# Performance work log

Measured on AMD Instinct MI355X. Metric: run time of the kernel, lower is better.

The kernel has to match this reference:

```python
import jax, jax.numpy as jnp
import numpy as np

TOP_K = 2
E = 8      # num_experts
D = 1024   # model dim
F = 2048   # expert hidden dim = int(2*3072/3), already a multiple of 256
B, S = 2, 1024


def setup_inputs() -> dict:
    key = jax.random.key(0)
    ks = jax.random.split(key, 8)
    sc = 0.02
    return {
        "x_bsD": jax.random.normal(ks[0], (B, S, D), dtype=jnp.float32),
        "router_DE": jax.random.normal(ks[1], (D, E), dtype=jnp.float32) * sc,
        "w_in_shared_FD": jax.random.normal(ks[2], (F, D), dtype=jnp.float32) * sc,
        "w_out_shared_DF": jax.random.normal(ks[3], (D, F), dtype=jnp.float32) * sc,
        "w_swiglu_FD": jax.random.normal(ks[4], (F, D), dtype=jnp.float32) * sc,
        "w_in_eDF": jax.random.normal(ks[5], (E, D, F), dtype=jnp.float32) * sc,
        "w_swiglu_eDF": jax.random.normal(ks[6], (E, D, F), dtype=jnp.float32) * sc,
        "w_out_eFD": jax.random.normal(ks[7], (E, F, D), dtype=jnp.float32) * sc,
    }


def reference(x_bsD, router_DE, w_in_shared_FD, w_out_shared_DF, w_swiglu_FD,
              w_in_eDF, w_swiglu_eDF, w_out_eFD):
    b, s, d = x_bsD.shape
    x_aD = x_bsD.reshape(-1, d)                      # [a, D]
    a = x_aD.shape[0]

    # Router (token choice): top-k per token, others masked to -inf
    scores_aE = x_aD @ router_DE                      # [a, E]
    topv_aK, topi_aK = jax.lax.top_k(scores_aE, TOP_K)
    masked_aE = jnp.full_like(scores_aE, -jnp.inf)
    masked_aE = masked_aE.at[jnp.arange(a)[:, None], topi_aK].set(topv_aK)
    # sigmoid(-inf) == 0 -> non-selected (expert, token) pairs contribute nothing
    gates_Ea = jax.nn.sigmoid(masked_aE.astype(jnp.float32)).astype(x_aD.dtype).T  # [E, a]

    # Dispatch: router_indices_EG == arange(a) per expert, so gather == broadcast
    routed_in_EaD = x_aD[None, :, :] * gates_Ea[:, :, None]   # [E, a, D]
    routed_in_EaD = jax.lax.stop_gradient(routed_in_EaD)      # matches .detach()

    # Per-expert bmm SwiGLU
    mid_EaF = jnp.einsum('ead,edf->eaf', routed_in_EaD, w_in_eDF)
    sw_EaF = jnp.einsum('ead,edf->eaf', routed_in_EaD, w_swiglu_eDF)
    h_EaF = jax.nn.silu(mid_EaF) * sw_EaF
    out_EaD = jnp.einsum('eaf,efd->ead', h_EaF, w_out_eFD)

    # Shared expert (computed under torch.no_grad in the original)
    shared_aF = jax.nn.silu(x_aD @ w_in_shared_FD.T) * (x_aD @ w_swiglu_FD.T)
    shared_out_aD = jax.lax.stop_gradient(shared_aF @ w_out_shared_DF.T)

    # Combine: scatter_add with per-expert arange indices == sum over experts
    out_aD = shared_out_aD + jnp.sum(out_EaD, axis=0)
    return out_aD.reshape(b, s, d)
```

## Files before the change

### kernel.cpp

```cpp
#include <hip/hip_runtime.h>
#include <hip/hip_bf16.h>

#define A_TOK 2048
#define DDIM 1024
#define FDIM 2048
#define NEXP 8
#define NE9 9
#define SLOTS_R (2 * A_TOK)
#define SLOTS_T (SLOTS_R + A_TOK)
#define NB1 (2 * FDIM)

#define PREP_TRA_END 4096
#define PREP_SH12_END (PREP_TRA_END + 1024)
#define PREP_SHOUT_END (PREP_SH12_END + 512)
#define PREP_NWG (PREP_SHOUT_END + 512)

typedef __attribute__((ext_vector_type(8))) short short8v;
typedef __attribute__((ext_vector_type(4))) float f32x4;
typedef __attribute__((ext_vector_type(4))) ushort ushort4v;

#define BARRIER() asm volatile("s_barrier" ::: "memory")
#define VMCNT(n) asm volatile("s_waitcnt vmcnt(" #n ")" ::: "memory")

__device__ __forceinline__ void lds16(const void* g, void* l) {
  __builtin_amdgcn_global_load_lds((const __attribute__((address_space(1))) void*)g,
                                   (__attribute__((address_space(3))) void*)l, 16, 0, 0);
}

__device__ __forceinline__ float sigmoidf_(float x) { return 1.f / (1.f + __expf(-x)); }
__device__ __forceinline__ ushort f2bf(float x) {
  __hip_bfloat16 b = __float2bfloat16(x);
  ushort u; __builtin_memcpy(&u, &b, 2); return u;
}
__device__ __forceinline__ float bf2f(ushort u) {
  union { unsigned int i; float f; } x; x.i = (unsigned int)u << 16; return x.f;
}

__global__ void k_prep(const float* __restrict__ w_in_e, const float* __restrict__ w_sw_e,
                       const float* __restrict__ w_in_sh, const float* __restrict__ w_sw_sh,
                       const float* __restrict__ w_out_sh,
                       ushort* __restrict__ wt12, ushort* __restrict__ wt_out_t,
                       const float* __restrict__ x, const float* __restrict__ rw,
                       __hip_bfloat16* __restrict__ xbf, int* __restrict__ top_e,
                       float* __restrict__ top_g) {
  __shared__ ushort tile[128][68];
  int b = blockIdx.x, tid = threadIdx.x;
  if (b < PREP_TRA_END) {
    int z = b >> 8, p = b & 255;
    int e = z & 7, which = z >> 3;
    const float* in = (which ? w_sw_e : w_in_e) + (size_t)e * DDIM * FDIM;
    ushort* outb = wt12 + (size_t)e * NB1 * DDIM;
    int r0 = (p & 7) * 128, c0 = (p >> 3) * 64;
    int rr = tid >> 4, cq = tid & 15;
    float4 va[8];
#pragma unroll
    for (int i = 0; i < 8; i++)
      va[i] = *(const float4*)(in + (size_t)(r0 + i * 16 + rr) * FDIM + c0 + cq * 4);
#pragma unroll
    for (int i = 0; i < 8; i++) {
      float4 v = va[i];
      ushort4v o = {f2bf(v.x), f2bf(v.y), f2bf(v.z), f2bf(v.w)};
      *(ushort4v*)&tile[i * 16 + rr][cq * 4] = o;
    }
    __syncthreads();
    int cc = tid >> 5, rq = tid & 31;
#pragma unroll
    for (int i = 0; i < 8; i++) {
      int c = i * 8 + cc;
      int f = c0 + c;
      int rp = ((f >> 5) << 6) + (which << 5) + (f & 31);
      ushort4v o = {tile[rq * 4 + 0][c], tile[rq * 4 + 1][c],
                    tile[rq * 4 + 2][c], tile[rq * 4 + 3][c]};
      *(ushort4v*)(outb + (size_t)rp * DDIM + r0 + rq * 4) = o;
    }
  } else if (b < PREP_SH12_END) {
    int j = b - PREP_TRA_END;
    int rj = j * 4 + (tid >> 6);
    int l = tid & 63;
    int which = rj & 1, f = rj >> 1;
    const float* src = (which ? w_sw_sh : w_in_sh) + (size_t)f * DDIM;
    int rp = ((f >> 5) << 6) + (which << 5) + (f & 31);
    ushort* dst = wt12 + (size_t)NEXP * NB1 * DDIM + (size_t)rp * DDIM;
#pragma unroll
    for (int i = 0; i < 4; i++) {
      int q = l + 64 * i;
      float4 v = ((const float4*)src)[q];
      ushort4v o = {f2bf(v.x), f2bf(v.y), f2bf(v.z), f2bf(v.w)};
      ((ushort4v*)dst)[q] = o;
    }
  } else if (b < PREP_SHOUT_END) {
    int j = b - PREP_SH12_END;
    int d = j * 2 + (tid >> 7);
    int l = tid & 127;
    const float* src = w_out_sh + (size_t)d * FDIM;
    ushort* dst = wt_out_t + (size_t)NEXP * DDIM * FDIM + (size_t)d * FDIM;
#pragma unroll
    for (int i = 0; i < 4; i++) {
      int q = l + 128 * i;
      float4 v = ((const float4*)src)[q];
      ushort4v o = {f2bf(v.x), f2bf(v.y), f2bf(v.z), f2bf(v.w)};
      ((ushort4v*)dst)[q] = o;
    }
  } else {
    int j = b - PREP_SHOUT_END;
    int t = j * 4 + (tid >> 6);
    int l = tid & 63;
    const float* xr = x + (size_t)t * DDIM;
    float acc[NEXP];
#pragma unroll
    for (int e = 0; e < NEXP; e++) acc[e] = 0.f;
#pragma unroll
    for (int i = 0; i < 16; i++) {
      int d = i * 64 + l;
      float v = xr[d];
      xbf[(size_t)t * DDIM + d] = __float2bfloat16(v);
      const float* rr = rw + (size_t)d * NEXP;
#pragma unroll
      for (int e = 0; e < NEXP; e++) acc[e] += v * rr[e];
    }
#pragma unroll
    for (int e = 0; e < NEXP; e++) {
#pragma unroll
      for (int s = 32; s > 0; s >>= 1) acc[e] += __shfl_xor(acc[e], s);
    }
    if (l == 0) {
      float b1 = -1e30f, b2 = -1e30f;
      int i1 = 0, i2 = 0;
#pragma unroll
      for (int e = 0; e < NEXP; e++) {
        float v = acc[e];
        if (v > b1) { b2 = b1; i2 = i1; b1 = v; i1 = e; }
        else if (v > b2) { b2 = v; i2 = e; }
      }
      top_e[t * 2 + 0] = i1; top_e[t * 2 + 1] = i2;
      top_g[t * 2 + 0] = sigmoidf_(b1); top_g[t * 2 + 1] = sigmoidf_(b2);
    }
  }
}

__global__ void k_scan(const int* __restrict__ top_e, int* __restrict__ counts,
                       int* __restrict__ offs, int* __restrict__ cursor) {
  __shared__ int hist[NEXP];
  int tid = threadIdx.x;
  if (tid < NEXP) hist[tid] = 0;
  __syncthreads();
  for (int i = tid; i < A_TOK * 2; i += 256) atomicAdd(&hist[top_e[i]], 1);
  __syncthreads();
  if (tid == 0) {
    int s = 0;
    for (int e = 0; e < NEXP; e++) { counts[e] = hist[e]; offs[e] = s; s += hist[e]; cursor[e] = 0; }
    counts[NEXP] = A_TOK;
    offs[NEXP] = s;
  }
}

__global__ void k_dispatch(const float* __restrict__ x, const int* __restrict__ top_e,
                           const float* __restrict__ top_g, const int* __restrict__ offs,
                           int* __restrict__ cursor, int* __restrict__ slot_of,
                           __hip_bfloat16* __restrict__ y) {
  int t = blockIdx.x * 4 + (threadIdx.x >> 6);
  int l = threadIdx.x & 63;
  int e0 = top_e[t * 2 + 0], e1 = top_e[t * 2 + 1];
  float g0 = top_g[t * 2 + 0], g1 = top_g[t * 2 + 1];
  int s0 = 0, s1 = 0;
  if (l == 0) {
    s0 = offs[e0] + atomicAdd(&cursor[e0], 1);
    s1 = offs[e1] + atomicAdd(&cursor[e1], 1);
    slot_of[t * 2 + 0] = s0; slot_of[t * 2 + 1] = s1;
  }
  s0 = __shfl(s0, 0); s1 = __shfl(s1, 0);
  const float* xr = x + (size_t)t * DDIM;
#pragma unroll
  for (int i = 0; i < 16; i++) {
    int d = i * 64 + l;
    float v = xr[d];
    y[(size_t)s0 * DDIM + d] = __float2bfloat16(v * g0);
    y[(size_t)s1 * DDIM + d] = __float2bfloat16(v * g1);
  }
}

__global__ __launch_bounds__(256, 3) void k_mlp1(
    const ushort* __restrict__ Abase, const ushort* __restrict__ Bbase,
    ushort* __restrict__ Obase, const int* __restrict__ d_cnt,
    const int* __restrict__ d_off, const float* __restrict__ w_out_e,
    ushort* __restrict__ wt_out_t) {
  constexpr int K = DDIM, NT = DDIM / 32;
  constexpr int BUF = 16384;
  __shared__ __align__(16) char smem[3 * BUF];
  int z = blockIdx.z;
  int tid = threadIdx.x;
  if (z < 4) {
    ushort (*tile)[68] = (ushort(*)[68])smem;
    int jj = (z * 16 + blockIdx.y) * 32 + blockIdx.x;
    int ex = jj >> 8, p = jj & 255;
    const float* in = w_out_e + (size_t)ex * FDIM * DDIM;
    ushort* outp = wt_out_t + (size_t)ex * DDIM * FDIM;
    int r0 = (p >> 4) * 128, c0 = (p & 15) * 64;
    int rr = tid >> 4, cq = tid & 15;
    float4 va[8];
#pragma unroll
    for (int i = 0; i < 8; i++)
      va[i] = *(const float4*)(in + (size_t)(r0 + i * 16 + rr) * DDIM + c0 + cq * 4);
#pragma unroll
    for (int i = 0; i < 8; i++) {
      float4 v = va[i];
      ushort4v o = {f2bf(v.x), f2bf(v.y), f2bf(v.z), f2bf(v.w)};
      *(ushort4v*)&tile[i * 16 + rr][cq * 4] = o;
    }
    __syncthreads();
    int cc = tid >> 5, rq = tid & 31;
#pragma unroll
    for (int i = 0; i < 8; i++) {
      int c = i * 8 + cc;
      ushort4v o = {tile[rq * 4 + 0][c], tile[rq * 4 + 1][c],
                    tile[rq * 4 + 2][c], tile[rq * 4 + 3][c]};
      *(ushort4v*)(outp + (size_t)(c0 + c) * FDIM + r0 + rq * 4) = o;
    }
    return;
  }
  int e = z - 4;
  int cnt = d_cnt[e];
  int m0 = blockIdx.y * 128;
  if (m0 >= cnt) return;
  int roff = d_off[e];
  int n0 = blockIdx.x * 128;
  const ushort* B = Bbase + (size_t)e * NB1 * DDIM;
  int w = tid >> 6, l = tid & 63;
  int wm = w >> 1, wn = w & 1, lr = l & 15, kg = l >> 4;
  size_t arow0 = (size_t)roff + m0;

  int srow = tid >> 2;
  int sgg = (tid & 3) ^ ((tid >> 3) & 3);
  const ushort* pA0 = Abase + (arow0 + srow) * (size_t)K + sgg * 8;
  const ushort* pA1 = pA0 + (size_t)64 * K;
  const ushort* pB0 = B + ((size_t)n0 + srow) * K + sgg * 8;
  const ushort* pB1 = pB0 + (size_t)64 * K;
  int tls = tid * 16;

  int xorg = (kg ^ ((lr >> 1) & 3)) << 4;
  int offA[4], offB[4];
#pragma unroll
  for (int i = 0; i < 4; i++) {
    offA[i] = (wm * 64 + i * 16 + lr) * 64 + xorg;
    offB[i] = 8192 + (wn * 64 + i * 16 + lr) * 64 + xorg;
  }

  f32x4 acc[4][4];
#pragma unroll
  for (int i = 0; i < 4; i++)
#pragma unroll
    for (int j = 0; j < 4; j++) acc[i][j] = {0.f, 0.f, 0.f, 0.f};

#pragma unroll
  for (int pt = 0; pt < 2; ++pt) {
    char* bb = smem + pt * BUF;
    lds16(pA0, bb + tls);         pA0 += 32;
    lds16(pA1, bb + 4096 + tls);  pA1 += 32;
    lds16(pB0, bb + 8192 + tls);  pB0 += 32;
    lds16(pB1, bb + 12288 + tls); pB1 += 32;
  }
  VMCNT(4);
  BARRIER();

  char* b0 = smem;
  char* b1 = smem + BUF;
  char* b2 = smem + 2 * BUF;
  for (int t = 0; t < NT; ++t) {
    bool st = (t + 2) < NT;
    short8v af[4], bf[4];
#pragma unroll
    for (int mf = 0; mf < 4; mf++) af[mf] = *(const short8v*)(b0 + offA[mf]);
#pragma unroll
    for (int nf = 0; nf < 2; nf++) bf[nf] = *(const short8v*)(b0 + offB[nf]);
    if (st) {
      lds16(pA0, b2 + tls);
      lds16(pA1, b2 + 4096 + tls);
    }
    pA0 += 32; pA1 += 32;
    BARRIER();
    __builtin_amdgcn_s_setprio(1);
#pragma unroll
    for (int nf = 0; nf < 2; nf++)
#pragma unroll
      for (int mf = 0; mf < 4; mf++)
        acc[mf][nf] = __builtin_amdgcn_mfma_f32_16x16x32_bf16(af[mf], bf[nf], acc[mf][nf], 0, 0, 0);
    __builtin_amdgcn_s_setprio(0);
    BARRIER();
#pragma unroll
    for (int nf = 2; nf < 4; nf++) bf[nf] = *(const short8v*)(b0 + offB[nf]);
    if (st) {
      lds16(pB0, b2 + 8192 + tls);
      lds16(pB1, b2 + 12288 + tls);
    }
    pB0 += 32; pB1 += 32;
    BARRIER();
    __builtin_amdgcn_s_setprio(1);
#pragma unroll
    for (int nf = 2; nf < 4; nf++)
#pragma unroll
      for (int mf = 0; mf < 4; mf++)
        acc[mf][nf] = __builtin_amdgcn_mfma_f32_16x16x32_bf16(af[mf], bf[nf], acc[mf][nf], 0, 0, 0);
    __builtin_amdgcn_s_setprio(0);
    if (t < NT - 1) {
      if (st) { VMCNT(4); } else { VMCNT(0); }
      BARRIER();
    }
    char* tmp = b0; b0 = b1; b1 = b2; b2 = tmp;
  }

  int j = (n0 >> 6) + wn;
#pragma unroll
  for (int mf = 0; mf < 4; mf++)
#pragma unroll
    for (int nf = 0; nf < 2; nf++)
#pragma unroll
      for (int r = 0; r < 4; r++) {
        int row = m0 + wm * 64 + mf * 16 + kg * 4 + r;
        if (row < cnt) {
          float mid = acc[mf][nf][r];
          float sw = acc[mf][nf + 2][r];
          float hv = mid * sigmoidf_(mid) * sw;
          int col = j * 32 + nf * 16 + lr;
          Obase[((size_t)roff + row) * FDIM + col] = f2bf(hv);
        }
      }
}

__global__ __launch_bounds__(256, 3) void k_mlp2(
    const ushort* __restrict__ Abase, const ushort* __restrict__ Bbase,
    ushort* __restrict__ part, const int* __restrict__ d_cnt,
    const int* __restrict__ d_off) {
  constexpr int K = FDIM, NT = 1024 / 32;
  constexpr int BUF = 16384;
  __shared__ __align__(16) char smem[3 * BUF];
  int e = blockIdx.z;
  int cnt = d_cnt[e];
  int mt = blockIdx.y >> 1, kz = blockIdx.y & 1;
  int m0 = mt * 128;
  if (m0 >= cnt) return;
  int roff = d_off[e];
  int n0 = blockIdx.x * 128;
  int kbeg = kz * 1024;
  const ushort* B = Bbase + (size_t)e * DDIM * FDIM;
  int tid = threadIdx.x, w = tid >> 6, l = tid & 63;
  int wm = w >> 1, wn = w & 1, lr = l & 15, kg = l >> 4;
  size_t arow0 = (size_t)roff + m0;

  int srow = tid >> 2;
  int sgg = (tid & 3) ^ ((tid >> 3) & 3);
  const ushort* pA0 = Abase + (arow0 + srow) * (size_t)K + kbeg + sgg * 8;
  const ushort* pA1 = pA0 + (size_t)64 * K;
  const ushort* pB0 = B + ((size_t)n0 + srow) * K + kbeg + sgg * 8;
  const ushort* pB1 = pB0 + (size_t)64 * K;
  int tls = tid * 16;

  int xorg = (kg ^ ((lr >> 1) & 3)) << 4;
  int offA[4], offB[4];
#pragma unroll
  for (int i = 0; i < 4; i++) {
    offA[i] = (wm * 64 + i * 16 + lr) * 64 + xorg;
    offB[i] = 8192 + (wn * 64 + i * 16 + lr) * 64 + xorg;
  }

  f32x4 acc[4][4];
#pragma unroll
  for (int i = 0; i < 4; i++)
#pragma unroll
    for (int j = 0; j < 4; j++) acc[i][j] = {0.f, 0.f, 0.f, 0.f};

#pragma unroll
  for (int pt = 0; pt < 2; ++pt) {
    char* bb = smem + pt * BUF;
    lds16(pA0, bb + tls);         pA0 += 32;
    lds16(pA1, bb + 4096 + tls);  pA1 += 32;
    lds16(pB0, bb + 8192 + tls);  pB0 += 32;
    lds16(pB1, bb + 12288 + tls); pB1 += 32;
  }
  VMCNT(4);
  BARRIER();

  char* b0 = smem;
  char* b1 = smem + BUF;
  char* b2 = smem + 2 * BUF;
  for (int t = 0; t < NT; ++t) {
    bool st = (t + 2) < NT;
    short8v af[4], bf[4];
#pragma unroll
    for (int mf = 0; mf < 4; mf++) af[mf] = *(const short8v*)(b0 + offA[mf]);
#pragma unroll
    for (int nf = 0; nf < 2; nf++) bf[nf] = *(const short8v*)(b0 + offB[nf]);
    if (st) {
      lds16(pA0, b2 + tls);
      lds16(pA1, b2 + 4096 + tls);
    }
    pA0 += 32; pA1 += 32;
    BARRIER();
    __builtin_amdgcn_s_setprio(1);
#pragma unroll
    for (int nf = 0; nf < 2; nf++)
#pragma unroll
      for (int mf = 0; mf < 4; mf++)
        acc[mf][nf] = __builtin_amdgcn_mfma_f32_16x16x32_bf16(af[mf], bf[nf], acc[mf][nf], 0, 0, 0);
    __builtin_amdgcn_s_setprio(0);
    BARRIER();
#pragma unroll
    for (int nf = 2; nf < 4; nf++) bf[nf] = *(const short8v*)(b0 + offB[nf]);
    if (st) {
      lds16(pB0, b2 + 8192 + tls);
      lds16(pB1, b2 + 12288 + tls);
    }
    pB0 += 32; pB1 += 32;
    BARRIER();
    __builtin_amdgcn_s_setprio(1);
#pragma unroll
    for (int nf = 2; nf < 4; nf++)
#pragma unroll
      for (int mf = 0; mf < 4; mf++)
        acc[mf][nf] = __builtin_amdgcn_mfma_f32_16x16x32_bf16(af[mf], bf[nf], acc[mf][nf], 0, 0, 0);
    __builtin_amdgcn_s_setprio(0);
    if (t < NT - 1) {
      if (st) { VMCNT(4); } else { VMCNT(0); }
      BARRIER();
    }
    char* tmp = b0; b0 = b1; b1 = b2; b2 = tmp;
  }

  ushort* outp = part + (size_t)kz * SLOTS_T * DDIM;
#pragma unroll
  for (int mf = 0; mf < 4; mf++)
#pragma unroll
    for (int nf = 0; nf < 4; nf++)
#pragma unroll
      for (int r = 0; r < 4; r++) {
        int row = m0 + wm * 64 + mf * 16 + kg * 4 + r;
        if (row < cnt) {
          int col = n0 + wn * 64 + nf * 16 + lr;
          outp[((size_t)roff + row) * DDIM + col] = f2bf(acc[mf][nf][r]);
        }
      }
}

__global__ void k_combine(const ushort* __restrict__ part, const int* __restrict__ slot_of,
                          float* __restrict__ out) {
  int t = blockIdx.x, q = threadIdx.x;
  int rows[3];
  rows[0] = slot_of[t * 2 + 0];
  rows[1] = slot_of[t * 2 + 1];
  rows[2] = SLOTS_R + t;
  size_t P = (size_t)SLOTS_T * DDIM;
  float o[4] = {0.f, 0.f, 0.f, 0.f};
#pragma unroll
  for (int kz = 0; kz < 2; kz++)
#pragma unroll
    for (int i = 0; i < 3; i++) {
      ushort4v v = *(const ushort4v*)(part + kz * P + (size_t)rows[i] * DDIM + q * 4);
#pragma unroll
      for (int j = 0; j < 4; j++) o[j] += bf2f(v[j]);
    }
  float4 ov = {o[0], o[1], o[2], o[3]};
  ((float4*)out)[(size_t)t * (DDIM / 4) + q] = ov;
}

extern "C" void kernel_launch(void* const* d_in, const int* in_sizes, int n_in,
                              void* d_out, int out_size, void* d_ws, size_t ws_size,
                              hipStream_t stream) {
  (void)in_sizes; (void)n_in; (void)out_size; (void)ws_size;
  const float* x        = (const float*)d_in[0];
  const float* router   = (const float*)d_in[1];
  const float* w_in_sh  = (const float*)d_in[2];
  const float* w_out_sh = (const float*)d_in[3];
  const float* w_sw_sh  = (const float*)d_in[4];
  const float* w_in_e   = (const float*)d_in[5];
  const float* w_sw_e   = (const float*)d_in[6];
  const float* w_out_e  = (const float*)d_in[7];
  float* out = (float*)d_out;

  char* ws = (char*)d_ws;
  size_t off = 0;
  auto alloc = [&](size_t bytes) -> char* {
    char* p = ws + off;
    off += (bytes + 255) & ~(size_t)255;
    return p;
  };
  ushort* wt12     = (ushort*)alloc((size_t)NE9 * NB1 * DDIM * 2);
  ushort* wt_out_t = (ushort*)alloc((size_t)NE9 * DDIM * FDIM * 2);
  __hip_bfloat16* y_all = (__hip_bfloat16*)alloc((size_t)SLOTS_R * DDIM * 2);
  __hip_bfloat16* xbf   = (__hip_bfloat16*)alloc((size_t)A_TOK * DDIM * 2);
  ushort* h        = (ushort*)alloc((size_t)SLOTS_T * FDIM * 2);
  int*   counts  = (int*)alloc(64);
  int*   offs    = (int*)alloc(64);
  int*   cursor  = (int*)alloc(64);
  int*   top_e   = (int*)alloc((size_t)A_TOK * 2 * 4);
  float* top_g   = (float*)alloc((size_t)A_TOK * 2 * 4);
  int*   slot_of = (int*)alloc((size_t)A_TOK * 2 * 4);
  (void)alloc(1 << 20);
  ushort* part = wt12;

  k_prep<<<dim3(PREP_NWG), 256, 0, stream>>>(
      w_in_e, w_sw_e, w_in_sh, w_sw_sh, w_out_sh,
      wt12, wt_out_t, x, router, xbf, top_e, top_g);

  k_scan<<<dim3(1), 256, 0, stream>>>(top_e, counts, offs, cursor);

  k_dispatch<<<dim3(A_TOK / 4), 256, 0, stream>>>(x, top_e, top_g, offs, cursor, slot_of, y_all);

  k_mlp1<<<dim3(NB1 / 128, A_TOK / 128, 4 + NE9), 256, 0, stream>>>(
      (const ushort*)y_all, wt12, h, counts, offs, w_out_e, wt_out_t);

  k_mlp2<<<dim3(DDIM / 128, (A_TOK / 128) * 2, NE9), 256, 0, stream>>>(
      h, wt_out_t, part, counts, offs);

  k_combine<<<dim3(A_TOK), 256, 0, stream>>>(part, slot_of, out);
}
```

Baseline: 248.9 us.

## Retile expert up-projection GEMM to 128x256 with 64-wide K steps

The expert up-projection kernel moves from 128x128 tiles with 256 threads and 32-wide K steps to 128x256 tiles with 512 threads (8 waves) and 64-wide K steps. It keeps triple-buffered LDS at 48KB per stage and uses a new 8-way XOR swizzle. The w_out_e fp32-to-bf16 transpose moves out of the GEMM launch into the prep kernel, so the GEMM grid no longer carries extra non-GEMM blocks. The goal is more reuse per byte loaded into LDS and fewer barriers per unit of K. In exchange, the ~144KB of LDS limits each CU to a single block, and the larger tile leaves fewer blocks to spread across CUs.

```diff
diff --git a/kernel.cpp b/kernel.cpp
--- a/kernel.cpp
+++ b/kernel.cpp
@@ -11,7 +11,8 @@
 #define NB1 (2 * FDIM)
 
 #define PREP_TRA_END 4096
-#define PREP_SH12_END (PREP_TRA_END + 1024)
+#define PREP_TRB_END (PREP_TRA_END + 2048)
+#define PREP_SH12_END (PREP_TRB_END + 1024)
 #define PREP_SHOUT_END (PREP_SH12_END + 512)
 #define PREP_NWG (PREP_SHOUT_END + 512)
 
@@ -37,8 +38,8 @@
 }
 
 __global__ void k_prep(const float* __restrict__ w_in_e, const float* __restrict__ w_sw_e,
-                       const float* __restrict__ w_in_sh, const float* __restrict__ w_sw_sh,
-                       const float* __restrict__ w_out_sh,
+                       const float* __restrict__ w_out_e, const float* __restrict__ w_in_sh,
+                       const float* __restrict__ w_sw_sh, const float* __restrict__ w_out_sh,
                        ushort* __restrict__ wt12, ushort* __restrict__ wt_out_t,
                        const float* __restrict__ x, const float* __restrict__ rw,
                        __hip_bfloat16* __restrict__ xbf, int* __restrict__ top_e,
@@ -73,8 +74,34 @@
                     tile[rq * 4 + 2][c], tile[rq * 4 + 3][c]};
       *(ushort4v*)(outb + (size_t)rp * DDIM + r0 + rq * 4) = o;
     }
+  } else if (b < PREP_TRB_END) {
+    int b2 = b - PREP_TRA_END;
+    int ex = b2 >> 8, p = b2 & 255;
+    const float* in = w_out_e + (size_t)ex * FDIM * DDIM;
+    ushort* outp = wt_out_t + (size_t)ex * DDIM * FDIM;
+    int r0 = (p >> 4) * 128, c0 = (p & 15) * 64;
+    int rr = tid >> 4, cq = tid & 15;
+    float4 va[8];
+#pragma unroll
+    for (int i = 0; i < 8; i++)
+      va[i] = *(const float4*)(in + (size_t)(r0 + i * 16 + rr) * DDIM + c0 + cq * 4);
+#pragma unroll
+    for (int i = 0; i < 8; i++) {
+      float4 v = va[i];
+      ushort4v o = {f2bf(v.x), f2bf(v.y), f2bf(v.z), f2bf(v.w)};
+      *(ushort4v*)&tile[i * 16 + rr][cq * 4] = o;
+    }
+    __syncthreads();
+    int cc = tid >> 5, rq = tid & 31;
+#pragma unroll
+    for (int i = 0; i < 8; i++) {
+      int c = i * 8 + cc;
+      ushort4v o = {tile[rq * 4 + 0][c], tile[rq * 4 + 1][c],
+                    tile[rq * 4 + 2][c], tile[rq * 4 + 3][c]};
+      *(ushort4v*)(outp + (size_t)(c0 + c) * FDIM + r0 + rq * 4) = o;
+    }
   } else if (b < PREP_SH12_END) {
-    int j = b - PREP_TRA_END;
+    int j = b - PREP_TRB_END;
     int rj = j * 4 + (tid >> 6);
     int l = tid & 63;
     int which = rj & 1, f = rj >> 1;
@@ -179,71 +206,42 @@
   }
 }
 
-__global__ __launch_bounds__(256, 3) void k_mlp1(
+__global__ __launch_bounds__(512, 1) void k_mlp1(
     const ushort* __restrict__ Abase, const ushort* __restrict__ Bbase,
     ushort* __restrict__ Obase, const int* __restrict__ d_cnt,
-    const int* __restrict__ d_off, const float* __restrict__ w_out_e,
-    ushort* __restrict__ wt_out_t) {
-  constexpr int K = DDIM, NT = DDIM / 32;
-  constexpr int BUF = 16384;
+    const int* __restrict__ d_off) {
+  constexpr int K = DDIM, NT = DDIM / 64;
+  constexpr int ABUF = 16384, BUF = 49152;
   __shared__ __align__(16) char smem[3 * BUF];
-  int z = blockIdx.z;
-  int tid = threadIdx.x;
-  if (z < 4) {
-    ushort (*tile)[68] = (ushort(*)[68])smem;
-    int jj = (z * 16 + blockIdx.y) * 32 + blockIdx.x;
-    int ex = jj >> 8, p = jj & 255;
-    const float* in = w_out_e + (size_t)ex * FDIM * DDIM;
-    ushort* outp = wt_out_t + (size_t)ex * DDIM * FDIM;
-    int r0 = (p >> 4) * 128, c0 = (p & 15) * 64;
-    int rr = tid >> 4, cq = tid & 15;
-    float4 va[8];
-#pragma unroll
-    for (int i = 0; i < 8; i++)
-      va[i] = *(const float4*)(in + (size_t)(r0 + i * 16 + rr) * DDIM + c0 + cq * 4);
-#pragma unroll
-    for (int i = 0; i < 8; i++) {
-      float4 v = va[i];
-      ushort4v o = {f2bf(v.x), f2bf(v.y), f2bf(v.z), f2bf(v.w)};
-      *(ushort4v*)&tile[i * 16 + rr][cq * 4] = o;
-    }
-    __syncthreads();
-    int cc = tid >> 5, rq = tid & 31;
-#pragma unroll
-    for (int i = 0; i < 8; i++) {
-      int c = i * 8 + cc;
-      ushort4v o = {tile[rq * 4 + 0][c], tile[rq * 4 + 1][c],
-                    tile[rq * 4 + 2][c], tile[rq * 4 + 3][c]};
-      *(ushort4v*)(outp + (size_t)(c0 + c) * FDIM + r0 + rq * 4) = o;
-    }
-    return;
-  }
-  int e = z - 4;
+  int e = blockIdx.z;
   int cnt = d_cnt[e];
   int m0 = blockIdx.y * 128;
   if (m0 >= cnt) return;
   int roff = d_off[e];
-  int n0 = blockIdx.x * 128;
+  int n0 = blockIdx.x * 256;
   const ushort* B = Bbase + (size_t)e * NB1 * DDIM;
-  int w = tid >> 6, l = tid & 63;
-  int wm = w >> 1, wn = w & 1, lr = l & 15, kg = l >> 4;
+  int tid = threadIdx.x, w = tid >> 6, l = tid & 63;
+  int wm = w >> 2, wn = w & 3, lr = l & 15, kg = l >> 4;
   size_t arow0 = (size_t)roff + m0;
 
-  int srow = tid >> 2;
-  int sgg = (tid & 3) ^ ((tid >> 3) & 3);
-  const ushort* pA0 = Abase + (arow0 + srow) * (size_t)K + sgg * 8;
+  int srow = tid >> 3;
+  int sg = (tid & 7) ^ (srow & 7);
+  const ushort* pA0 = Abase + (arow0 + srow) * (size_t)K + sg * 8;
   const ushort* pA1 = pA0 + (size_t)64 * K;
-  const ushort* pB0 = B + ((size_t)n0 + srow) * K + sgg * 8;
+  const ushort* pB0 = B + ((size_t)n0 + srow) * K + sg * 8;
   const ushort* pB1 = pB0 + (size_t)64 * K;
+  const ushort* pB2 = pB0 + (size_t)128 * K;
+  const ushort* pB3 = pB0 + (size_t)192 * K;
   int tls = tid * 16;
 
-  int xorg = (kg ^ ((lr >> 1) & 3)) << 4;
   int offA[4], offB[4];
 #pragma unroll
   for (int i = 0; i < 4; i++) {
-    offA[i] = (wm * 64 + i * 16 + lr) * 64 + xorg;
-    offB[i] = 8192 + (wn * 64 + i * 16 + lr) * 64 + xorg;
-  }
+    offA[i] = (wm * 64 + i * 16 + lr) * 128;
+    offB[i] = ABUF + (wn * 64 + i * 16 + lr) * 128;
+  }
+  int sk0 = (kg ^ (lr & 7)) << 4;
+  int sk1 = ((4 + kg) ^ (lr & 7)) << 4;
 
   f32x4 acc[4][4];
 #pragma unroll
@@ -254,12 +252,14 @@
 #pragma unroll
   for (int pt = 0; pt < 2; ++pt) {
     char* bb = smem + pt * BUF;
-    lds16(pA0, bb + tls);         pA0 += 32;
-    lds16(pA1, bb + 4096 + tls);  pA1 += 32;
-    lds16(pB0, bb + 8192 + tls);  pB0 += 32;
-    lds16(pB1, bb + 12288 + tls); pB1 += 32;
-  }
-  VMCNT(4);
+    lds16(pA0, bb + tls);                pA0 += 64;
+    lds16(pA1, bb + 8192 + tls);         pA1 += 64;
+    lds16(pB0, bb + ABUF + tls);         pB0 += 64;
+    lds16(pB1, bb + ABUF + 8192 + tls);  pB1 += 64;
+    lds16(pB2, bb + ABUF + 16384 + tls); pB2 += 64;
+    lds16(pB3, bb + ABUF + 24576 + tls); pB3 += 64;
+  }
+  VMCNT(6);
   BARRIER();
 
   char* b0 = smem;
@@ -269,14 +269,11 @@
     bool st = (t + 2) < NT;
     short8v af[4], bf[4];
 #pragma unroll
-    for (int mf = 0; mf < 4; mf++) af[mf] = *(const short8v*)(b0 + offA[mf]);
-#pragma unroll
-    for (int nf = 0; nf < 2; nf++) bf[nf] = *(const short8v*)(b0 + offB[nf]);
-    if (st) {
-      lds16(pA0, b2 + tls);
-      lds16(pA1, b2 + 4096 + tls);
-    }
-    pA0 += 32; pA1 += 32;
+    for (int i = 0; i < 4; i++) af[i] = *(const short8v*)(b0 + offA[i] + sk0);
+    bf[0] = *(const short8v*)(b0 + offB[0] + sk0);
+    bf[1] = *(const short8v*)(b0 + offB[1] + sk0);
+    if (st) { lds16(pA0, b2 + tls); lds16(pA1, b2 + 8192 + tls); }
+    pA0 += 64; pA1 += 64;
     BARRIER();
     __builtin_amdgcn_s_setprio(1);
 #pragma unroll
@@ -286,13 +283,10 @@
         acc[mf][nf] = __builtin_amdgcn_mfma_f32_16x16x32_bf16(af[mf], bf[nf], acc[mf][nf], 0, 0, 0);
     __builtin_amdgcn_s_setprio(0);
     BARRIER();
-#pragma unroll
-    for (int nf = 2; nf < 4; nf++) bf[nf] = *(const short8v*)(b0 + offB[nf]);
-    if (st) {
-      lds16(pB0, b2 + 8192 + tls);
-      lds16(pB1, b2 + 12288 + tls);
-    }
-    pB0 += 32; pB1 += 32;
+    bf[2] = *(const short8v*)(b0 + offB[2] + sk0);
+    bf[3] = *(const short8v*)(b0 + offB[3] + sk0);
+    if (st) { lds16(pB0, b2 + ABUF + tls); lds16(pB1, b2 + ABUF + 8192 + tls); }
+    pB0 += 64; pB1 += 64;
     BARRIER();
     __builtin_amdgcn_s_setprio(1);
 #pragma unroll
@@ -301,10 +295,34 @@
       for (int mf = 0; mf < 4; mf++)
         acc[mf][nf] = __builtin_amdgcn_mfma_f32_16x16x32_bf16(af[mf], bf[nf], acc[mf][nf], 0, 0, 0);
     __builtin_amdgcn_s_setprio(0);
-    if (t < NT - 1) {
-      if (st) { VMCNT(4); } else { VMCNT(0); }
-      BARRIER();
-    }
+    BARRIER();
+#pragma unroll
+    for (int i = 0; i < 4; i++) af[i] = *(const short8v*)(b0 + offA[i] + sk1);
+    bf[0] = *(const short8v*)(b0 + offB[0] + sk1);
+    bf[1] = *(const short8v*)(b0 + offB[1] + sk1);
+    if (st) { lds16(pB2, b2 + ABUF + 16384 + tls); lds16(pB3, b2 + ABUF + 24576 + tls); }
+    pB2 += 64; pB3 += 64;
+    BARRIER();
+    __builtin_amdgcn_s_setprio(1);
+#pragma unroll
+    for (int nf = 0; nf < 2; nf++)
+#pragma unroll
+      for (int mf = 0; mf < 4; mf++)
+        acc[mf][nf] = __builtin_amdgcn_mfma_f32_16x16x32_bf16(af[mf], bf[nf], acc[mf][nf], 0, 0, 0);
+    __builtin_amdgcn_s_setprio(0);
+    BARRIER();
+    bf[2] = *(const short8v*)(b0 + offB[2] + sk1);
+    bf[3] = *(const short8v*)(b0 + offB[3] + sk1);
+    if (st) { VMCNT(6); } else { VMCNT(0); }
+    BARRIER();
+    __builtin_amdgcn_s_setprio(1);
+#pragma unroll
+    for (int nf = 2; nf < 4; nf++)
+#pragma unroll
+      for (int mf = 0; mf < 4; mf++)
+        acc[mf][nf] = __builtin_amdgcn_mfma_f32_16x16x32_bf16(af[mf], bf[nf], acc[mf][nf], 0, 0, 0);
+    __builtin_amdgcn_s_setprio(0);
+    BARRIER();
     char* tmp = b0; b0 = b1; b1 = b2; b2 = tmp;
   }
 
@@ -497,15 +515,15 @@
   ushort* part = wt12;
 
   k_prep<<<dim3(PREP_NWG), 256, 0, stream>>>(
-      w_in_e, w_sw_e, w_in_sh, w_sw_sh, w_out_sh,
+      w_in_e, w_sw_e, w_out_e, w_in_sh, w_sw_sh, w_out_sh,
       wt12, wt_out_t, x, router, xbf, top_e, top_g);
 
   k_scan<<<dim3(1), 256, 0, stream>>>(top_e, counts, offs, cursor);
 
   k_dispatch<<<dim3(A_TOK / 4), 256, 0, stream>>>(x, top_e, top_g, offs, cursor, slot_of, y_all);
 
-  k_mlp1<<<dim3(NB1 / 128, A_TOK / 128, 4 + NE9), 256, 0, stream>>>(
-      (const ushort*)y_all, wt12, h, counts, offs, w_out_e, wt_out_t);
+  k_mlp1<<<dim3(NB1 / 256, A_TOK / 128, NE9), 512, 0, stream>>>(
+      (const ushort*)y_all, wt12, h, counts, offs);
 
   k_mlp2<<<dim3(DDIM / 128, (A_TOK / 128) * 2, NE9), 256, 0, stream>>>(
       h, wt_out_t, part, counts, offs);
```

New measurement: 259.8 us. 1.04x slower.

## Move w_out transpose into prep kernel and remap block orders for XCD locality

Applied to the files above, without the earlier changes.

Moves the per-expert w_out fp32→bf16 transpose out of the GEMM1 launch, where it ran as extra z-slices, into the prep kernel as a new block range. It also remaps prep block indices and GEMM1 n-tile indices so that consecutive hardware blocks, which are spread round-robin across XCDs, touch related data. The aim is to remove the heterogeneous transpose blocks from the GEMM grid and improve L2 locality per XCD. The cost is a larger prep kernel that now serially carries all weight conversion before dispatch.

```diff
diff --git a/kernel.cpp b/kernel.cpp
--- a/kernel.cpp
+++ b/kernel.cpp
@@ -11,7 +11,8 @@
 #define NB1 (2 * FDIM)
 
 #define PREP_TRA_END 4096
-#define PREP_SH12_END (PREP_TRA_END + 1024)
+#define PREP_TRB_END (PREP_TRA_END + 2048)
+#define PREP_SH12_END (PREP_TRB_END + 1024)
 #define PREP_SHOUT_END (PREP_SH12_END + 512)
 #define PREP_NWG (PREP_SHOUT_END + 512)
 
@@ -37,14 +38,15 @@
 }
 
 __global__ void k_prep(const float* __restrict__ w_in_e, const float* __restrict__ w_sw_e,
-                       const float* __restrict__ w_in_sh, const float* __restrict__ w_sw_sh,
-                       const float* __restrict__ w_out_sh,
+                       const float* __restrict__ w_out_e, const float* __restrict__ w_in_sh,
+                       const float* __restrict__ w_sw_sh, const float* __restrict__ w_out_sh,
                        ushort* __restrict__ wt12, ushort* __restrict__ wt_out_t,
                        const float* __restrict__ x, const float* __restrict__ rw,
                        __hip_bfloat16* __restrict__ xbf, int* __restrict__ top_e,
                        float* __restrict__ top_g) {
   __shared__ ushort tile[128][68];
-  int b = blockIdx.x, tid = threadIdx.x;
+  int b = (blockIdx.x & 7) * (PREP_NWG / 8) + (blockIdx.x >> 3);
+  int tid = threadIdx.x;
   if (b < PREP_TRA_END) {
     int z = b >> 8, p = b & 255;
     int e = z & 7, which = z >> 3;
@@ -73,8 +75,34 @@
                     tile[rq * 4 + 2][c], tile[rq * 4 + 3][c]};
       *(ushort4v*)(outb + (size_t)rp * DDIM + r0 + rq * 4) = o;
     }
+  } else if (b < PREP_TRB_END) {
+    int b2 = b - PREP_TRA_END;
+    int ex = b2 >> 8, p = b2 & 255;
+    const float* in = w_out_e + (size_t)ex * FDIM * DDIM;
+    ushort* outp = wt_out_t + (size_t)ex * DDIM * FDIM;
+    int r0 = (p & 15) * 128, c0 = (p >> 4) * 64;
+    int rr = tid >> 4, cq = tid & 15;
+    float4 va[8];
+#pragma unroll
+    for (int i = 0; i < 8; i++)
+      va[i] = *(const float4*)(in + (size_t)(r0 + i * 16 + rr) * DDIM + c0 + cq * 4);
+#pragma unroll
+    for (int i = 0; i < 8; i++) {
+      float4 v = va[i];
+      ushort4v o = {f2bf(v.x), f2bf(v.y), f2bf(v.z), f2bf(v.w)};
+      *(ushort4v*)&tile[i * 16 + rr][cq * 4] = o;
+    }
+    __syncthreads();
+    int cc = tid >> 5, rq = tid & 31;
+#pragma unroll
+    for (int i = 0; i < 8; i++) {
+      int c = i * 8 + cc;
+      ushort4v o = {tile[rq * 4 + 0][c], tile[rq * 4 + 1][c],
+                    tile[rq * 4 + 2][c], tile[rq * 4 + 3][c]};
+      *(ushort4v*)(outp + (size_t)(c0 + c) * FDIM + r0 + rq * 4) = o;
+    }
   } else if (b < PREP_SH12_END) {
-    int j = b - PREP_TRA_END;
+    int j = b - PREP_TRB_END;
     int rj = j * 4 + (tid >> 6);
     int l = tid & 63;
     int which = rj & 1, f = rj >> 1;
@@ -182,50 +210,18 @@
 __global__ __launch_bounds__(256, 3) void k_mlp1(
     const ushort* __restrict__ Abase, const ushort* __restrict__ Bbase,
     ushort* __restrict__ Obase, const int* __restrict__ d_cnt,
-    const int* __restrict__ d_off, const float* __restrict__ w_out_e,
-    ushort* __restrict__ wt_out_t) {
+    const int* __restrict__ d_off) {
   constexpr int K = DDIM, NT = DDIM / 32;
   constexpr int BUF = 16384;
   __shared__ __align__(16) char smem[3 * BUF];
-  int z = blockIdx.z;
-  int tid = threadIdx.x;
-  if (z < 4) {
-    ushort (*tile)[68] = (ushort(*)[68])smem;
-    int jj = (z * 16 + blockIdx.y) * 32 + blockIdx.x;
-    int ex = jj >> 8, p = jj & 255;
-    const float* in = w_out_e + (size_t)ex * FDIM * DDIM;
-    ushort* outp = wt_out_t + (size_t)ex * DDIM * FDIM;
-    int r0 = (p >> 4) * 128, c0 = (p & 15) * 64;
-    int rr = tid >> 4, cq = tid & 15;
-    float4 va[8];
-#pragma unroll
-    for (int i = 0; i < 8; i++)
-      va[i] = *(const float4*)(in + (size_t)(r0 + i * 16 + rr) * DDIM + c0 + cq * 4);
-#pragma unroll
-    for (int i = 0; i < 8; i++) {
-      float4 v = va[i];
-      ushort4v o = {f2bf(v.x), f2bf(v.y), f2bf(v.z), f2bf(v.w)};
-      *(ushort4v*)&tile[i * 16 + rr][cq * 4] = o;
-    }
-    __syncthreads();
-    int cc = tid >> 5, rq = tid & 31;
-#pragma unroll
-    for (int i = 0; i < 8; i++) {
-      int c = i * 8 + cc;
-      ushort4v o = {tile[rq * 4 + 0][c], tile[rq * 4 + 1][c],
-                    tile[rq * 4 + 2][c], tile[rq * 4 + 3][c]};
-      *(ushort4v*)(outp + (size_t)(c0 + c) * FDIM + r0 + rq * 4) = o;
-    }
-    return;
-  }
-  int e = z - 4;
+  int e = blockIdx.z;
   int cnt = d_cnt[e];
   int m0 = blockIdx.y * 128;
   if (m0 >= cnt) return;
   int roff = d_off[e];
-  int n0 = blockIdx.x * 128;
+  int n0 = (((blockIdx.x & 7) << 2) + (blockIdx.x >> 3)) * 128;
   const ushort* B = Bbase + (size_t)e * NB1 * DDIM;
-  int w = tid >> 6, l = tid & 63;
+  int tid = threadIdx.x, w = tid >> 6, l = tid & 63;
   int wm = w >> 1, wn = w & 1, lr = l & 15, kg = l >> 4;
   size_t arow0 = (size_t)roff + m0;
 
@@ -497,15 +493,15 @@
   ushort* part = wt12;
 
   k_prep<<<dim3(PREP_NWG), 256, 0, stream>>>(
-      w_in_e, w_sw_e, w_in_sh, w_sw_sh, w_out_sh,
+      w_in_e, w_sw_e, w_out_e, w_in_sh, w_sw_sh, w_out_sh,
       wt12, wt_out_t, x, router, xbf, top_e, top_g);
 
   k_scan<<<dim3(1), 256, 0, stream>>>(top_e, counts, offs, cursor);
 
   k_dispatch<<<dim3(A_TOK / 4), 256, 0, stream>>>(x, top_e, top_g, offs, cursor, slot_of, y_all);
 
-  k_mlp1<<<dim3(NB1 / 128, A_TOK / 128, 4 + NE9), 256, 0, stream>>>(
-      (const ushort*)y_all, wt12, h, counts, offs, w_out_e, wt_out_t);
+  k_mlp1<<<dim3(NB1 / 128, A_TOK / 128, NE9), 256, 0, stream>>>(
+      (const ushort*)y_all, wt12, h, counts, offs);
 
   k_mlp2<<<dim3(DDIM / 128, (A_TOK / 128) * 2, NE9), 256, 0, stream>>>(
       h, wt_out_t, part, counts, offs);
```

Result: no change. 252.2 us (+1.3%).
